# Performance work log

Hardware: AMD Instinct MI355X
Metric: run time of the kernel (lower is better)

The kernel has to match this reference:

```python
import jax, jax.numpy as jnp
import numpy as np

H = 50  # LSTM units
T = 10  # NUMBARS
F = 5   # input features
B = 131072


def _lstm(x, W, U, b):
    """Keras-default LSTM. x: [B,T,Fin], W: [Fin,4H], U: [H,4H], b: [4H].
    Gate order i,f,g(c),o; sigmoid recurrent act, tanh cell act, zero init state.
    Returns (all_h [B,T,H], last_h [B,H])."""
    Bn = x.shape[0]
    h0 = jnp.zeros((Bn, H), x.dtype)
    c0 = jnp.zeros((Bn, H), x.dtype)

    def step(carry, xt):
        h, c = carry
        z = xt @ W + h @ U + b  # [B,4H]
        i, f, g, o = jnp.split(z, 4, axis=-1)
        i = jax.nn.sigmoid(i)
        f = jax.nn.sigmoid(f)
        g = jnp.tanh(g)
        o = jax.nn.sigmoid(o)
        c_new = f * c + i * g
        h_new = o * jnp.tanh(c_new)
        return (h_new, c_new), h_new

    (h_last, _), hs = jax.lax.scan(step, (h0, c0), jnp.swapaxes(x, 0, 1))
    return jnp.swapaxes(hs, 0, 1), h_last


def setup_inputs() -> dict:
    key = jax.random.key(0)
    ks = jax.random.split(key, 16)
    d = {"x": jax.random.normal(ks[0], (B, T, F), dtype=jnp.float32)}
    in_dims = [F, H, H, H]
    for l in range(4):
        s_in = 1.0 / np.sqrt(in_dims[l])
        s_h = 1.0 / np.sqrt(H)
        d[f"W{l+1}"] = jax.random.normal(ks[1 + 3 * l], (in_dims[l], 4 * H), dtype=jnp.float32) * s_in
        d[f"U{l+1}"] = jax.random.normal(ks[2 + 3 * l], (H, 4 * H), dtype=jnp.float32) * s_h
        # Keras unit_forget_bias: forget-gate bias = 1
        b = jnp.zeros((4 * H,), jnp.float32).at[H:2 * H].set(1.0)
        d[f"b{l+1}"] = b
    d["Wd1"] = jax.random.normal(ks[13], (H, 50), dtype=jnp.float32) * (1.0 / np.sqrt(H))
    d["bd1"] = jnp.zeros((50,), jnp.float32)
    d["Wd2"] = jax.random.normal(ks[14], (50, 1), dtype=jnp.float32) * (1.0 / np.sqrt(50))
    d["bd2"] = jnp.zeros((1,), jnp.float32)
    return d


def reference(x, W1, U1, b1, W2, U2, b2, W3, U3, b3, W4, U4, b4, Wd1, bd1, Wd2, bd2):
    # Dropout layers are identity at inference (Keras default training=False).
    h, _ = _lstm(x, W1, U1, b1)
    h, _ = _lstm(h, W2, U2, b2)
    h, _ = _lstm(h, W3, U3, b3)
    _, h = _lstm(h, W4, U4, b4)        # return_sequences=False -> last h [B,H]
    h = h @ Wd1 + bd1                   # Dense(50), linear activation
    out = jax.nn.sigmoid(h @ Wd2 + bd2) # Dense(1, sigmoid) -> [B,1]
    return out
```

## Files before the change

kernel.cpp:

```cpp
#include <hip/hip_runtime.h>


typedef __attribute__((ext_vector_type(8))) short short8;
typedef __attribute__((ext_vector_type(4))) float floatx4;
typedef __attribute__((ext_vector_type(2))) float float2v;
typedef unsigned short u16;
typedef unsigned int u32;

constexpr int H_ = 50, T_ = 10, F_ = 5;
constexpr int MTILE = 32;
constexpr int BLKT = 256;
constexpr float LOG2E = 1.4426950408889634f;

__device__ __forceinline__ float rcp_(float x) { return __builtin_amdgcn_rcpf(x); }
__device__ __forceinline__ float exp2_(float x) { return __builtin_amdgcn_exp2f(x); }
__device__ __forceinline__ float sig_nat(float x) {
  return rcp_(1.0f + exp2_(-LOG2E * x));
}

__device__ __forceinline__ u16 f2bf(float f) {
  union { float f; unsigned u; } v; v.f = f;
  unsigned r = v.u + 0x7FFFu + ((v.u >> 16) & 1u);
  return (u16)(r >> 16);
}
__device__ __forceinline__ float bf2f(u16 s) {
  union { unsigned u; float f; } v; v.u = ((unsigned)s) << 16;
  return v.f;
}
__device__ __forceinline__ unsigned cvt_pk_bf16(float lo, float hi) {
  unsigned r;
  asm("v_cvt_pk_bf16_f32 %0, %1, %2" : "=v"(r) : "v"(lo), "v"(hi));
  return r;
}

__global__ void prep_kernel(
    const float* W1, const float* U1, const float* b1, const float* W2,
    const float* U2, const float* b2, const float* W3, const float* U3,
    const float* b3, const float* W4, const float* U4, const float* b4,
    const float* Wd1, const float* bd1, const float* Wd2, const float* bd2,
    u16* Wpp, float* biasP, float* vdense) {
  int idx = blockIdx.x * blockDim.x + threadIdx.x;
  const float* Wt[4] = {W1, W2, W3, W4};
  const float* Ut[4] = {U1, U2, U3, U4};
  const float* bt[4] = {b1, b2, b3, b4};
  const int fin[4] = {F_, H_, H_, H_};
  if (idx < 4 * 32768) {
    int l = idx >> 15, r = idx & 32767;
    int j = r & 7, lane = (r >> 3) & 63, w = (r >> 9) & 3, gI = (r >> 11) & 3,
        kt = r >> 13;
    int row = kt * 32 + (lane >> 4) * 8 + j;
    int u = w * 16 + (lane & 15);
    float val = 0.0f;
    if (u < H_) {
      if (row < 64) {
        if (row < fin[l]) val = Wt[l][row * 200 + gI * H_ + u];
      } else {
        int rr = row - 64;
        if (rr < H_) val = Ut[l][rr * 200 + gI * H_ + u];
      }
    }
    val *= (gI == 2) ? (2.0f * LOG2E) : (-LOG2E);
    Wpp[idx] = f2bf(val);
  } else if (idx < 4 * 32768 + 1024) {
    int r = idx - 4 * 32768;
    int l = r >> 8, q = r & 255, gI = q >> 6, u = q & 63;
    float val = (u < H_) ? bt[l][gI * H_ + u] : 0.0f;
    biasP[r] = val * ((gI == 2) ? (2.0f * LOG2E) : (-LOG2E));
  } else if (idx < 4 * 32768 + 1024 + 51) {
    int u = idx - (4 * 32768 + 1024);
    if (u < H_) {
      float s = 0.0f;
      for (int n = 0; n < H_; ++n) s += Wd1[u * H_ + n] * Wd2[n];
      vdense[u] = s;
    } else {
      float s = bd2[0];
      for (int n = 0; n < H_; ++n) s += bd1[n] * Wd2[n];
      vdense[50] = s;
    }
  }
}

__global__ __launch_bounds__(BLKT, 4) void lstm_fused(
    const float* __restrict__ x0, const u16* __restrict__ Wpp,
    const float* __restrict__ biasP, const float* __restrict__ vdense,
    float* __restrict__ out) {
  __shared__ __align__(16) u16 buf[T_ * 2048];

  const int tid = threadIdx.x;
  const int w = tid >> 6, lane = tid & 63;
  const int np = lane & 15, quad = lane >> 4;
  const int b0 = blockIdx.x * MTILE;
  const int u = w * 16 + np;

  for (int i = tid; i < T_ * 1024; i += BLKT) ((u32*)buf)[i] = 0;
  __syncthreads();
  for (int e = tid; e < MTILE * 50; e += BLKT) {
    int row = e / 50, q = e - row * 50;
    int t = q / 5, f = q - t * 5;
    buf[t * 2048 + (row >> 4) * 1024 + (row & 15) * 8 + f] =
        f2bf(x0[(size_t)(b0 + row) * 50 + q]);
  }
  __syncthreads();

  const int rbase = quad * 128 + np * 8;
  const int cb0 = (w >> 1) * 512 + ((w & 1) * 2 + (np >> 3)) * 128 + quad * 32 + (np & 7);

  float2v cst[4];

#pragma unroll 1
  for (int l = 0; l < 4; ++l) {
    const u16* wp = Wpp + l * 32768;
    short8 bfr[4][4];
#pragma unroll
    for (int kt = 0; kt < 4; ++kt)
#pragma unroll
      for (int g = 0; g < 4; ++g)
        bfr[kt][g] = *(const short8*)&wp[(((kt * 4 + g) * 4 + w) * 64 + lane) * 8];
    float bv[4];
#pragma unroll
    for (int g = 0; g < 4; ++g) bv[g] = biasP[l * 256 + g * 64 + u];
#pragma unroll
    for (int i = 0; i < 4; ++i) cst[i] = float2v{0.0f, 0.0f};

#pragma unroll 1
    for (int t = 0; t < T_; ++t) {
      u16* bt = &buf[t * 2048];
      const u16* bp = &buf[(t == 0 ? 0 : (t - 1)) * 2048];

      floatx4 acc[2][4];
#pragma unroll
      for (int mt = 0; mt < 2; ++mt)
#pragma unroll
        for (int g = 0; g < 4; ++g)
          acc[mt][g] = floatx4{bv[g], bv[g], bv[g], bv[g]};

#pragma unroll
      for (int mt = 0; mt < 2; ++mt) {
        short8 a0 = *(const short8*)&bt[mt * 1024 + rbase];
#pragma unroll
        for (int g = 0; g < 4; ++g)
          acc[mt][g] = __builtin_amdgcn_mfma_f32_16x16x32_bf16(
              a0, bfr[0][g], acc[mt][g], 0, 0, 0);
        if (l > 0) {
          short8 a1 = *(const short8*)&bt[mt * 1024 + 512 + rbase];
#pragma unroll
          for (int g = 0; g < 4; ++g)
            acc[mt][g] = __builtin_amdgcn_mfma_f32_16x16x32_bf16(
                a1, bfr[1][g], acc[mt][g], 0, 0, 0);
        }
      }
      if (t > 0) {
#pragma unroll
        for (int mt = 0; mt < 2; ++mt) {
          short8 h0 = *(const short8*)&bp[mt * 1024 + rbase];
          short8 h1 = *(const short8*)&bp[mt * 1024 + 512 + rbase];
#pragma unroll
          for (int g = 0; g < 4; ++g) {
            acc[mt][g] = __builtin_amdgcn_mfma_f32_16x16x32_bf16(
                h0, bfr[2][g], acc[mt][g], 0, 0, 0);
            acc[mt][g] = __builtin_amdgcn_mfma_f32_16x16x32_bf16(
                h1, bfr[3][g], acc[mt][g], 0, 0, 0);
          }
        }
      }
      __syncthreads();

#pragma unroll
      for (int mt = 0; mt < 2; ++mt) {
#pragma unroll
        for (int p = 0; p < 2; ++p) {
          float2v di = {exp2_(acc[mt][0][2 * p]), exp2_(acc[mt][0][2 * p + 1])};
          float2v df = {exp2_(acc[mt][1][2 * p]), exp2_(acc[mt][1][2 * p + 1])};
          float2v dg = {exp2_(acc[mt][2][2 * p]), exp2_(acc[mt][2][2 * p + 1])};
          float2v do_ = {exp2_(acc[mt][3][2 * p]), exp2_(acc[mt][3][2 * p + 1])};
          di += 1.0f; df += 1.0f; dg += 1.0f; do_ += 1.0f;
          float2v m1 = di * df, m2 = do_ * dg;
          float2v P = m1 * m2;
          float Rs = rcp_(P.x * P.y);
          float2v R = {Rs * P.y, Rs * P.x};
          float2v i_ = (df * m2) * R;
          float2v f_ = (di * m2) * R;
          float2v o_ = (m1 * dg) * R;
          float2v g_ = 1.0f - 2.0f * ((m1 * do_) * R);
          float2v cn = f_ * cst[mt * 2 + p] + i_ * g_;
          cst[mt * 2 + p] = cn;
          float2v s = cn * (2.0f * LOG2E);
          float2v dc = {exp2_(s.x), exp2_(s.y)};
          dc += 1.0f;
          float Rc = rcp_(dc.x * dc.y);
          float2v tc = 1.0f - 2.0f * float2v{Rc * dc.y, Rc * dc.x};
          float2v h = o_ * tc;
          unsigned pk = cvt_pk_bf16(h.x, h.y);
          int a0 = cb0 + mt * 1024 + p * 16;
          bt[a0] = (u16)pk;
          bt[a0 + 8] = (u16)(pk >> 16);
        }
      }
      __syncthreads();
    }
  }

  if (tid < MTILE) {
    int mt = tid >> 4, rr = tid & 15;
    const u16* b9 = &buf[9 * 2048];
    float s = vdense[50];
    for (int k = 0; k < H_; ++k) {
      int kk = k >> 5, qd = (k & 31) >> 3, j = k & 7;
      s += bf2f(b9[mt * 1024 + kk * 512 + qd * 128 + rr * 8 + j]) * vdense[k];
    }
    out[b0 + tid] = sig_nat(s);
  }
}

extern "C" void kernel_launch(void* const* d_in, const int* in_sizes, int n_in,
                              void* d_out, int out_size, void* d_ws,
                              size_t ws_size, hipStream_t stream) {
  const float* x = (const float*)d_in[0];
  const float* W1 = (const float*)d_in[1];
  const float* U1 = (const float*)d_in[2];
  const float* b1 = (const float*)d_in[3];
  const float* W2 = (const float*)d_in[4];
  const float* U2 = (const float*)d_in[5];
  const float* b2 = (const float*)d_in[6];
  const float* W3 = (const float*)d_in[7];
  const float* U3 = (const float*)d_in[8];
  const float* b3 = (const float*)d_in[9];
  const float* W4 = (const float*)d_in[10];
  const float* U4 = (const float*)d_in[11];
  const float* b4 = (const float*)d_in[12];
  const float* Wd1 = (const float*)d_in[13];
  const float* bd1 = (const float*)d_in[14];
  const float* Wd2 = (const float*)d_in[15];
  const float* bd2 = (const float*)d_in[16];

  const int Bn = in_sizes[0] / (T_ * F_);
  const int nblk = Bn / MTILE;
  char* ws = (char*)d_ws;
  u16* Wpp = (u16*)ws;
  float* biasP = (float*)(ws + 262144);
  float* vdense = (float*)(ws + 262144 + 4096);
  float* out = (float*)d_out;

  prep_kernel<<<(4 * 32768 + 1024 + 51 + 255) / 256, 256, 0, stream>>>(
      W1, U1, b1, W2, U2, b2, W3, U3, b3, W4, U4, b4, Wd1, bd1, Wd2, bd2, Wpp,
      biasP, vdense);

  lstm_fused<<<dim3(nblk), dim3(BLKT), 0, stream>>>(x, Wpp, biasP, vdense, out);
}
```

Before: 491.9 us.

## Halve batch tile and drop one barrier per step via register prefetch

Each block now handles 16 batch rows instead of 32, so LDS use and per-wave accumulator state are halved. The occupancy hint in the launch bounds is lowered from 4 to 3. The next step's input fragment is loaded into registers before the new hidden state overwrites that slot, which removes one __syncthreads per timestep. The cost is twice as many blocks, each reloading the full weight fragments, and half the MFMA work per wave to hide the recurrent latency.

```diff
diff --git a/kernel.cpp b/kernel.cpp
--- a/kernel.cpp
+++ b/kernel.cpp
@@ -8,7 +8,7 @@
 typedef unsigned int u32;
 
 constexpr int H_ = 50, T_ = 10, F_ = 5;
-constexpr int MTILE = 32;
+constexpr int MTILE = 16;
 constexpr int BLKT = 256;
 constexpr float LOG2E = 1.4426950408889634f;
 
@@ -80,11 +80,11 @@
   }
 }
 
-__global__ __launch_bounds__(BLKT, 4) void lstm_fused(
+__global__ __launch_bounds__(BLKT, 3) void lstm_fused(
     const float* __restrict__ x0, const u16* __restrict__ Wpp,
     const float* __restrict__ biasP, const float* __restrict__ vdense,
     float* __restrict__ out) {
-  __shared__ __align__(16) u16 buf[T_ * 2048];
+  __shared__ __align__(16) u16 buf[T_ * 1024];
 
   const int tid = threadIdx.x;
   const int w = tid >> 6, lane = tid & 63;
@@ -92,20 +92,23 @@
   const int b0 = blockIdx.x * MTILE;
   const int u = w * 16 + np;
 
-  for (int i = tid; i < T_ * 1024; i += BLKT) ((u32*)buf)[i] = 0;
+  for (int i = tid; i < T_ * 512; i += BLKT) ((u32*)buf)[i] = 0;
   __syncthreads();
   for (int e = tid; e < MTILE * 50; e += BLKT) {
     int row = e / 50, q = e - row * 50;
     int t = q / 5, f = q - t * 5;
-    buf[t * 2048 + (row >> 4) * 1024 + (row & 15) * 8 + f] =
-        f2bf(x0[(size_t)(b0 + row) * 50 + q]);
+    buf[t * 1024 + row * 8 + f] = f2bf(x0[(size_t)(b0 + row) * 50 + q]);
   }
   __syncthreads();
 
   const int rbase = quad * 128 + np * 8;
   const int cb0 = (w >> 1) * 512 + ((w & 1) * 2 + (np >> 3)) * 128 + quad * 32 + (np & 7);
 
-  float2v cst[4];
+  float2v cst[2];
+
+  short8 xa0, xa1;
+  xa0 = *(const short8*)&buf[rbase];
+  xa1 = xa0;
 
 #pragma unroll 1
   for (int l = 0; l < 4; ++l) {
@@ -119,94 +122,89 @@
     float bv[4];
 #pragma unroll
     for (int g = 0; g < 4; ++g) bv[g] = biasP[l * 256 + g * 64 + u];
-#pragma unroll
-    for (int i = 0; i < 4; ++i) cst[i] = float2v{0.0f, 0.0f};
+    cst[0] = float2v{0.0f, 0.0f};
+    cst[1] = float2v{0.0f, 0.0f};
 
 #pragma unroll 1
     for (int t = 0; t < T_; ++t) {
-      u16* bt = &buf[t * 2048];
-      const u16* bp = &buf[(t == 0 ? 0 : (t - 1)) * 2048];
-
-      floatx4 acc[2][4];
-#pragma unroll
-      for (int mt = 0; mt < 2; ++mt)
+      u16* bt = &buf[t * 1024];
+      const u16* bp = &buf[(t == 0 ? 0 : (t - 1)) * 1024];
+
+      floatx4 acc[4];
+#pragma unroll
+      for (int g = 0; g < 4; ++g) acc[g] = floatx4{bv[g], bv[g], bv[g], bv[g]};
+
+#pragma unroll
+      for (int g = 0; g < 4; ++g)
+        acc[g] = __builtin_amdgcn_mfma_f32_16x16x32_bf16(xa0, bfr[0][g], acc[g],
+                                                         0, 0, 0);
+      if (l > 0) {
 #pragma unroll
         for (int g = 0; g < 4; ++g)
-          acc[mt][g] = floatx4{bv[g], bv[g], bv[g], bv[g]};
-
-#pragma unroll
-      for (int mt = 0; mt < 2; ++mt) {
-        short8 a0 = *(const short8*)&bt[mt * 1024 + rbase];
-#pragma unroll
-        for (int g = 0; g < 4; ++g)
-          acc[mt][g] = __builtin_amdgcn_mfma_f32_16x16x32_bf16(
-              a0, bfr[0][g], acc[mt][g], 0, 0, 0);
-        if (l > 0) {
-          short8 a1 = *(const short8*)&bt[mt * 1024 + 512 + rbase];
-#pragma unroll
-          for (int g = 0; g < 4; ++g)
-            acc[mt][g] = __builtin_amdgcn_mfma_f32_16x16x32_bf16(
-                a1, bfr[1][g], acc[mt][g], 0, 0, 0);
+          acc[g] = __builtin_amdgcn_mfma_f32_16x16x32_bf16(xa1, bfr[1][g],
+                                                           acc[g], 0, 0, 0);
+      }
+      if (t > 0) {
+        short8 h0 = *(const short8*)&bp[rbase];
+        short8 h1 = *(const short8*)&bp[512 + rbase];
+#pragma unroll
+        for (int g = 0; g < 4; ++g) {
+          acc[g] = __builtin_amdgcn_mfma_f32_16x16x32_bf16(h0, bfr[2][g], acc[g],
+                                                           0, 0, 0);
+          acc[g] = __builtin_amdgcn_mfma_f32_16x16x32_bf16(h1, bfr[3][g], acc[g],
+                                                           0, 0, 0);
         }
       }
-      if (t > 0) {
-#pragma unroll
-        for (int mt = 0; mt < 2; ++mt) {
-          short8 h0 = *(const short8*)&bp[mt * 1024 + rbase];
-          short8 h1 = *(const short8*)&bp[mt * 1024 + 512 + rbase];
-#pragma unroll
-          for (int g = 0; g < 4; ++g) {
-            acc[mt][g] = __builtin_amdgcn_mfma_f32_16x16x32_bf16(
-                h0, bfr[2][g], acc[mt][g], 0, 0, 0);
-            acc[mt][g] = __builtin_amdgcn_mfma_f32_16x16x32_bf16(
-                h1, bfr[3][g], acc[mt][g], 0, 0, 0);
-          }
-        }
+
+      if (t < T_ - 1) {
+        const u16* ns = &buf[(t + 1) * 1024];
+        xa0 = *(const short8*)&ns[rbase];
+        if (l > 0) xa1 = *(const short8*)&ns[512 + rbase];
+      } else if (l < 3) {
+        xa0 = *(const short8*)&buf[rbase];
+        xa1 = *(const short8*)&buf[512 + rbase];
+      }
+
+
+#pragma unroll
+      for (int p = 0; p < 2; ++p) {
+        float2v di = {exp2_(acc[0][2 * p]), exp2_(acc[0][2 * p + 1])};
+        float2v df = {exp2_(acc[1][2 * p]), exp2_(acc[1][2 * p + 1])};
+        float2v dg = {exp2_(acc[2][2 * p]), exp2_(acc[2][2 * p + 1])};
+        float2v do_ = {exp2_(acc[3][2 * p]), exp2_(acc[3][2 * p + 1])};
+        di += 1.0f; df += 1.0f; dg += 1.0f; do_ += 1.0f;
+        float2v m1 = di * df, m2 = do_ * dg;
+        float2v P = m1 * m2;
+        float Rs = rcp_(P.x * P.y);
+        float2v R = {Rs * P.y, Rs * P.x};
+        float2v i_ = (df * m2) * R;
+        float2v f_ = (di * m2) * R;
+        float2v o_ = (m1 * dg) * R;
+        float2v g_ = 1.0f - 2.0f * ((m1 * do_) * R);
+        float2v cn = f_ * cst[p] + i_ * g_;
+        cst[p] = cn;
+        float2v s = cn * (2.0f * LOG2E);
+        float2v dc = {exp2_(s.x), exp2_(s.y)};
+        dc += 1.0f;
+        float Rc = rcp_(dc.x * dc.y);
+        float2v tc = 1.0f - 2.0f * float2v{Rc * dc.y, Rc * dc.x};
+        float2v h = o_ * tc;
+        unsigned pk = cvt_pk_bf16(h.x, h.y);
+        int a0 = cb0 + p * 16;
+        bt[a0] = (u16)pk;
+        bt[a0 + 8] = (u16)(pk >> 16);
       }
       __syncthreads();
-
-#pragma unroll
-      for (int mt = 0; mt < 2; ++mt) {
-#pragma unroll
-        for (int p = 0; p < 2; ++p) {
-          float2v di = {exp2_(acc[mt][0][2 * p]), exp2_(acc[mt][0][2 * p + 1])};
-          float2v df = {exp2_(acc[mt][1][2 * p]), exp2_(acc[mt][1][2 * p + 1])};
-          float2v dg = {exp2_(acc[mt][2][2 * p]), exp2_(acc[mt][2][2 * p + 1])};
-          float2v do_ = {exp2_(acc[mt][3][2 * p]), exp2_(acc[mt][3][2 * p + 1])};
-          di += 1.0f; df += 1.0f; dg += 1.0f; do_ += 1.0f;
-          float2v m1 = di * df, m2 = do_ * dg;
-          float2v P = m1 * m2;
-          float Rs = rcp_(P.x * P.y);
-          float2v R = {Rs * P.y, Rs * P.x};
-          float2v i_ = (df * m2) * R;
-          float2v f_ = (di * m2) * R;
-          float2v o_ = (m1 * dg) * R;
-          float2v g_ = 1.0f - 2.0f * ((m1 * do_) * R);
-          float2v cn = f_ * cst[mt * 2 + p] + i_ * g_;
-          cst[mt * 2 + p] = cn;
-          float2v s = cn * (2.0f * LOG2E);
-          float2v dc = {exp2_(s.x), exp2_(s.y)};
-          dc += 1.0f;
-          float Rc = rcp_(dc.x * dc.y);
-          float2v tc = 1.0f - 2.0f * float2v{Rc * dc.y, Rc * dc.x};
-          float2v h = o_ * tc;
-          unsigned pk = cvt_pk_bf16(h.x, h.y);
-          int a0 = cb0 + mt * 1024 + p * 16;
-          bt[a0] = (u16)pk;
-          bt[a0 + 8] = (u16)(pk >> 16);
-        }
-      }
-      __syncthreads();
     }
   }
 
   if (tid < MTILE) {
-    int mt = tid >> 4, rr = tid & 15;
-    const u16* b9 = &buf[9 * 2048];
+    int rr = tid;
+    const u16* b9 = &buf[9 * 1024];
     float s = vdense[50];
     for (int k = 0; k < H_; ++k) {
       int kk = k >> 5, qd = (k & 31) >> 3, j = k & 7;
-      s += bf2f(b9[mt * 1024 + kk * 512 + qd * 128 + rr * 8 + j]) * vdense[k];
+      s += bf2f(b9[kk * 512 + qd * 128 + rr * 8 + j]) * vdense[k];
     }
     out[b0 + tid] = sig_nat(s);
   }
```

New measurement: 503.7 us. +2.4%, slower.
